# Kernel tuning notes

Hardware: AMD Instinct MI355X
Metric: run time of the kernel (lower is better)

## Reference

```python
import jax, jax.numpy as jnp
import numpy as np
import math

BS, QL, KL = 2, 2048, 2048
H, D = 16, 64          # n_heads, cell_dim
QS = KS = VS = 1024    # query/key/value feature sizes
HD = H * D


def setup_inputs() -> dict:
    key = jax.random.key(0)
    ks = jax.random.split(key, 12)
    s_in = 1.0 / math.sqrt(QS)
    s_hd = 1.0 / math.sqrt(HD)
    return {
        "query": jax.random.normal(ks[0], (BS, QL, QS), jnp.float32),
        "key": jax.random.normal(ks[1], (BS, KL, KS), jnp.float32),
        "value": jax.random.normal(ks[2], (BS, KL, VS), jnp.float32),
        # nn.Linear weights stored as [in, out] for x @ W + b
        "Wq_w": jax.random.normal(ks[3], (QS, HD), jnp.float32) * s_in,
        "Wq_b": jax.random.normal(ks[4], (HD,), jnp.float32) * s_in,
        "Wk_w": jax.random.normal(ks[5], (KS, HD), jnp.float32) * s_in,
        "Wk_b": jax.random.normal(ks[6], (HD,), jnp.float32) * s_in,
        "Wv_w": jax.random.normal(ks[7], (VS, HD), jnp.float32) * s_in,
        "Wv_b": jax.random.normal(ks[8], (HD,), jnp.float32) * s_in,
        "Wo_w": jax.random.normal(ks[9], (HD, HD), jnp.float32) * s_hd,
        "Wo_b": jax.random.normal(ks[10], (HD,), jnp.float32) * s_hd,
    }


def reference(query, key, value, Wq_w, Wq_b, Wk_w, Wk_b, Wv_w, Wv_b, Wo_w, Wo_b):
    bs, ql, _ = query.shape
    kl = key.shape[1]
    # project and split heads; torch .chunk along dim 2 == head-major reshape
    q = (query @ Wq_w + Wq_b).reshape(bs, ql, H, D).transpose(0, 2, 1, 3)  # bhqd
    k = (key @ Wk_w + Wk_b).reshape(bs, kl, H, D).transpose(0, 2, 1, 3)    # bhkd
    v = (value @ Wv_w + Wv_b).reshape(bs, kl, H, D).transpose(0, 2, 1, 3)  # bhkd
    scores = jnp.einsum("bhqd,bhkd->bhqk", q, k) / jnp.sqrt(jnp.float32(D))
    # log_softmax(...).exp() == softmax (use_mask=False path)
    w = jax.nn.softmax(scores, axis=-1)
    heads = jnp.einsum("bhqk,bhkd->bhqd", w, v)
    out = heads.transpose(0, 2, 1, 3).reshape(bs, ql, HD)  # concat heads on dim 2
    return out @ Wo_w + Wo_b
```

## Files before the change

kernel.cpp:

```cpp
#include <hip/hip_runtime.h>

#define BSZ 2
#define SEQ 2048
#define NH 16
#define DHD 64
#define HDIM 1024
#define FS 1024
#define MR (BSZ*SEQ)
#define L2E 1.4426950408889634f

typedef __bf16 bf16x8 __attribute__((ext_vector_type(8)));
typedef __bf16 bf16x2t __attribute__((ext_vector_type(2)));
typedef float f32x4 __attribute__((ext_vector_type(4)));
typedef float f32x16 __attribute__((ext_vector_type(16)));
typedef unsigned short u16;
typedef unsigned int u32;
typedef u32 u32x4 __attribute__((ext_vector_type(4)));

__device__ __forceinline__ u16 f2bf(float f) {
  u32 x = __float_as_uint(f);
  return (u16)((x + 0x7fffu + ((x >> 16) & 1u)) >> 16);
}

__device__ __forceinline__ u32 pack2bf(float a, float b) {
  bf16x2t t = {(__bf16)a, (__bf16)b};
  return __builtin_bit_cast(u32, t);
}

__device__ __forceinline__ void gload16(const void* g, void* l) {
  __builtin_amdgcn_global_load_lds(
      (const __attribute__((address_space(1))) u32*)g,
      (__attribute__((address_space(3))) u32*)l, 16, 0, 0);
}

__global__ __launch_bounds__(256) void transw4_k(
    const float* __restrict__ W0, const float* __restrict__ W1,
    const float* __restrict__ W2, const float* __restrict__ W3,
    u16* __restrict__ WTbase) {
  __shared__ float t[32][33];
  const int z = blockIdx.z;
  const float* W = z == 0 ? W0 : z == 1 ? W1 : z == 2 ? W2 : W3;
  u16* WT = WTbase + (size_t)z * FS * HDIM;
  const int tx = threadIdx.x, ty = threadIdx.y;
  const int c0 = blockIdx.x * 32, r0 = blockIdx.y * 32;
#pragma unroll
  for (int i = 0; i < 4; i++)
    t[ty + 8 * i][tx] = W[(size_t)(r0 + ty + 8 * i) * FS + c0 + tx];
  __syncthreads();
#pragma unroll
  for (int i = 0; i < 4; i++)
    WT[(size_t)(c0 + ty + 8 * i) * FS + r0 + tx] = f2bf(t[tx][ty + 8 * i]);
}

__global__ __launch_bounds__(256, 2) void gemmQKV_k(
    const float* __restrict__ qf32, const float* __restrict__ kf32,
    const float* __restrict__ vf32, const u16* __restrict__ WTbase,
    const float* __restrict__ bq, const float* __restrict__ bk,
    const float* __restrict__ bv, u16* __restrict__ QKbase,
    u16* __restrict__ VpT) {
  __shared__ u16 aL[2][128 * 64];
  __shared__ u16 bL[2][128 * 64];
  const int grp = blockIdx.y;
  const float* Af = grp == 0 ? qf32 : grp == 1 ? kf32 : vf32;
  const u16* BT = WTbase + (size_t)grp * FS * HDIM;
  const float* bias = grp == 0 ? bq : grp == 1 ? bk : bv;
  const int bx = blockIdx.x;
  const int m0 = (4 * (bx & 7) + (bx >> 6)) << 7;
  const int n0 = ((bx >> 3) & 7) << 7;
  const int tid = threadIdx.x, w = tid >> 6, lane = tid & 63;
  const int wr = ((w >> 1) << 6), wc = ((w & 1) << 6);
  const int li = lane & 15, g = lane >> 4;

  f32x4 acc[4][4];
#pragma unroll
  for (int i = 0; i < 4; i++)
#pragma unroll
    for (int j = 0; j < 4; j++) acc[i][j] = (f32x4){0.f, 0.f, 0.f, 0.f};

  const float* asrc[4];
  const u16* bsrc[4];
  int ldoff[4];
#pragma unroll
  for (int j = 0; j < 4; j++) {
    const int c = w * 4 + j;
    const int r = c * 8 + (lane >> 3);
    const int sc = (lane & 7) ^ (r & 7);
    asrc[j] = Af + (size_t)(m0 + r) * FS + sc * 8;
    bsrc[j] = BT + (size_t)(n0 + r) * FS + sc * 8;
    ldoff[j] = c * 1024;
  }

  float4 ar0[4], ar1[4];
#pragma unroll
  for (int j = 0; j < 4; j++) gload16(bsrc[j], (char*)bL[0] + ldoff[j]);
#pragma unroll
  for (int j = 0; j < 4; j++) {
    ar0[j] = *(const float4*)(asrc[j]);
    ar1[j] = *(const float4*)(asrc[j] + 4);
  }

  for (int kt = 0; kt < 16; kt++) {
    const int cur = kt & 1;
#pragma unroll
    for (int j = 0; j < 4; j++) {
      u32x4 pk;
      pk[0] = pack2bf(ar0[j].x, ar0[j].y);
      pk[1] = pack2bf(ar0[j].z, ar0[j].w);
      pk[2] = pack2bf(ar1[j].x, ar1[j].y);
      pk[3] = pack2bf(ar1[j].z, ar1[j].w);
      *(u32x4*)((char*)aL[cur] + ldoff[j] + lane * 16) = pk;
    }
    asm volatile("s_waitcnt lgkmcnt(0)" ::: "memory");
    __builtin_amdgcn_s_barrier();
    __builtin_amdgcn_sched_barrier(0);
    if (kt + 1 < 16) {
      const int ko = (kt + 1) * 64;
#pragma unroll
      for (int j = 0; j < 4; j++)
        gload16(bsrc[j] + ko, (char*)bL[cur ^ 1] + ldoff[j]);
#pragma unroll
      for (int j = 0; j < 4; j++) {
        ar0[j] = *(const float4*)(asrc[j] + ko);
        ar1[j] = *(const float4*)(asrc[j] + ko + 4);
      }
    }
    bf16x8 af[2][4], bfr[2][4];
#pragma unroll
    for (int ks = 0; ks < 2; ks++) {
#pragma unroll
      for (int mf = 0; mf < 4; mf++) {
        const int r = wr + mf * 16 + li;
        const int sl = (g + 4 * ks) ^ (r & 7);
        af[ks][mf] = *(const bf16x8*)((const char*)aL[cur] + r * 128 + sl * 16);
      }
#pragma unroll
      for (int nf = 0; nf < 4; nf++) {
        const int r = wc + nf * 16 + li;
        const int sl = (g + 4 * ks) ^ (r & 7);
        bfr[ks][nf] = *(const bf16x8*)((const char*)bL[cur] + r * 128 + sl * 16);
      }
    }
#pragma unroll
    for (int ks = 0; ks < 2; ks++)
#pragma unroll
      for (int mf = 0; mf < 4; mf++)
#pragma unroll
        for (int nf = 0; nf < 4; nf++)
          acc[mf][nf] = __builtin_amdgcn_mfma_f32_16x16x32_bf16(
              af[ks][mf], bfr[ks][nf], acc[mf][nf], 0, 0, 0);
  }

  if (grp < 2) {
    const float osc = grp == 0 ? 0.125f * L2E : 1.0f;
    u16* C = QKbase + (size_t)grp * MR * HDIM;
#pragma unroll
    for (int mf = 0; mf < 4; mf++)
#pragma unroll
      for (int nf = 0; nf < 4; nf++) {
        const int n = n0 + wc + nf * 16 + li;
        const float bvl = bias[n];
#pragma unroll
        for (int r4 = 0; r4 < 4; r4++) {
          const int m = m0 + wr + mf * 16 + g * 4 + r4;
          C[(size_t)m * HDIM + n] = f2bf((acc[mf][nf][r4] + bvl) * osc);
        }
      }
  } else {
#pragma unroll
    for (int mf = 0; mf < 4; mf++)
#pragma unroll
      for (int nf = 0; nf < 4; nf++) {
        const int n = n0 + wc + nf * 16 + li;
        const float bvl = bias[n];
        const int m = m0 + wr + mf * 16 + g * 4;
        const int bb = m >> 11, kv = m & 2047;
        ushort4 o;
        o.x = f2bf(acc[mf][nf][0] + bvl);
        o.y = f2bf(acc[mf][nf][1] + bvl);
        o.z = f2bf(acc[mf][nf][2] + bvl);
        o.w = f2bf(acc[mf][nf][3] + bvl);
        *(ushort4*)(VpT +
                    ((size_t)(bb * NH + (n >> 6)) * DHD + (n & 63)) * SEQ + kv) = o;
      }
  }
}

__global__ __launch_bounds__(256, 2) void gemm_out_k(
    const u16* __restrict__ A, const u16* __restrict__ BT,
    const float* __restrict__ bias, float* __restrict__ C) {
  __shared__ u16 aL[128 * 64];
  __shared__ u16 bL[128 * 64];
  const int bx = blockIdx.x;
  const int m0 = (4 * (bx & 7) + (bx >> 6)) << 7;
  const int n0 = ((bx >> 3) & 7) << 7;
  const int tid = threadIdx.x, w = tid >> 6, lane = tid & 63;
  const int wr = ((w >> 1) << 6), wc = ((w & 1) << 6);
  const int li = lane & 15, g = lane >> 4;

  f32x4 acc[4][4];
#pragma unroll
  for (int i = 0; i < 4; i++)
#pragma unroll
    for (int j = 0; j < 4; j++) acc[i][j] = (f32x4){0.f, 0.f, 0.f, 0.f};

  for (int k0 = 0; k0 < HDIM; k0 += 64) {
#pragma unroll
    for (int j = 0; j < 4; j++) {
      const int c = w * 4 + j;
      const int r = c * 8 + (lane >> 3);
      const int sc = (lane & 7) ^ (r & 7);
      gload16(A + (size_t)(m0 + r) * HDIM + k0 + sc * 8, (char*)aL + c * 1024);
      gload16(BT + (size_t)(n0 + r) * HDIM + k0 + sc * 8, (char*)bL + c * 1024);
    }
    __syncthreads();
    bf16x8 af[2][4], bfr[2][4];
#pragma unroll
    for (int ks = 0; ks < 2; ks++) {
#pragma unroll
      for (int mf = 0; mf < 4; mf++) {
        const int r = wr + mf * 16 + li;
        const int sl = (g + 4 * ks) ^ (r & 7);
        af[ks][mf] = *(const bf16x8*)((const char*)aL + r * 128 + sl * 16);
      }
#pragma unroll
      for (int nf = 0; nf < 4; nf++) {
        const int r = wc + nf * 16 + li;
        const int sl = (g + 4 * ks) ^ (r & 7);
        bfr[ks][nf] = *(const bf16x8*)((const char*)bL + r * 128 + sl * 16);
      }
    }
#pragma unroll
    for (int ks = 0; ks < 2; ks++)
#pragma unroll
      for (int mf = 0; mf < 4; mf++)
#pragma unroll
        for (int nf = 0; nf < 4; nf++)
          acc[mf][nf] = __builtin_amdgcn_mfma_f32_16x16x32_bf16(
              af[ks][mf], bfr[ks][nf], acc[mf][nf], 0, 0, 0);
    __syncthreads();
  }

#pragma unroll
  for (int mf = 0; mf < 4; mf++)
#pragma unroll
    for (int nf = 0; nf < 4; nf++) {
      const int n = n0 + wc + nf * 16 + li;
      const float bvl = bias[n];
#pragma unroll
      for (int r4 = 0; r4 < 4; r4++) {
        const int m = m0 + wr + mf * 16 + g * 4 + r4;
        C[(size_t)m * HDIM + n] = acc[mf][nf][r4] + bvl;
      }
    }
}

__global__ __launch_bounds__(512, 1) void attn_k(
    const u16* __restrict__ Qp, const u16* __restrict__ Kp,
    const u16* __restrict__ VpT, u16* __restrict__ Hd) {
  __shared__ u16 kbuf[4][64 * 64];
  __shared__ u16 vbuf[4][64 * 64];

  const int bid = blockIdx.x;
  const int swz = (bid & 7) * 64 + (bid >> 3);
  const int qb = swz & 15;
  const int h = (swz >> 4) & 15;
  const int b = swz >> 8;
  const int tid = threadIdx.x, w = tid >> 6, lane = tid & 63;
  const int sel = w >> 2, g3 = w & 3;
  const int q32 = lane & 31, hi = lane >> 5;
  const int q0 = qb << 7;
  const size_t qbase = (size_t)(b * SEQ + q0) * HDIM + (size_t)h * DHD;
  const size_t kbase = (size_t)(b * SEQ) * HDIM + (size_t)h * DHD;
  const size_t vtbase = (size_t)(b * NH + h) * DHD * SEQ;

  const int rr = lane >> 3;
  const int sc8 = ((lane & 7) ^ rr) * 8;
  const int fkey = (q32 & 7) << 4;

#pragma unroll
  for (int j = 0; j < 2; j++) {
    const int c = w * 2 + j;
    const int r = c * 8 + rr;
    gload16(Qp + qbase + (size_t)r * HDIM + sc8, (char*)kbuf + c * 1024);
  }
  __syncthreads();
  bf16x8 qf[4];
  {
    const char* qbp = (const char*)kbuf + (g3 * 32 + q32) * 128;
#pragma unroll
    for (int ds = 0; ds < 4; ds++)
      qf[ds] = *(const bf16x8*)(qbp + ((32 * ds + 16 * hi) ^ fkey));
  }
  __syncthreads();

  bf16x8 ones1;
#pragma unroll
  for (int i = 0; i < 8; i++) ones1[i] = (__bf16)1.0f;

  float mrun = -1e30f;
  f32x16 o0, o1, lacc;
#pragma unroll
  for (int i = 0; i < 16; i++) { o0[i] = 0.f; o1[i] = 0.f; lacc[i] = 0.f; }

  const int c0j = g3 * 2;
  const int r0r = c0j * 8 + rr;
  const u16* kp0 = Kp + kbase + (size_t)(r0r + sel * 64) * HDIM + sc8;
  const u16* kp1 = kp0 + (size_t)8 * HDIM;
  const u16* vp0 = VpT + vtbase + (size_t)r0r * SEQ + sel * 64 + sc8;
  const u16* vp1 = vp0 + (size_t)8 * SEQ;
  const int ldk0 = c0j * 1024, ldk1 = (c0j + 1) * 1024;

  auto stage2 = [&](int buf) {
    gload16(kp0, (char*)kbuf[buf] + ldk0);
    gload16(kp1, (char*)kbuf[buf] + ldk1);
    gload16(vp0, (char*)vbuf[buf] + ldk0);
    gload16(vp1, (char*)vbuf[buf] + ldk1);
    kp0 += (size_t)128 * HDIM;
    kp1 += (size_t)128 * HDIM;
    vp0 += 128;
    vp1 += 128;
  };

  stage2(sel);

#pragma unroll 1
  for (int p = 0; p < SEQ / 128; p++) {
    __syncthreads();
    if (p + 1 < SEQ / 128) stage2(sel + 2 * ((p + 1) & 1));
    const char* kl = (const char*)kbuf[sel + 2 * (p & 1)];
    const char* vl = (const char*)vbuf[sel + 2 * (p & 1)];

    f32x16 s0, s1;
#pragma unroll
    for (int i = 0; i < 16; i++) { s0[i] = 0.f; s1[i] = 0.f; }
#pragma unroll
    for (int ds = 0; ds < 4; ds++) {
      const int off = (32 * ds + 16 * hi) ^ fkey;
      const bf16x8 ka = *(const bf16x8*)(kl + q32 * 128 + off);
      const bf16x8 kb2 = *(const bf16x8*)(kl + (32 + q32) * 128 + off);
      s0 = __builtin_amdgcn_mfma_f32_32x32x16_bf16(ka, qf[ds], s0, 0, 0, 0);
      s1 = __builtin_amdgcn_mfma_f32_32x32x16_bf16(kb2, qf[ds], s1, 0, 0, 0);
    }

    float t0 = fmaxf(fmaxf(s0[0], s0[1]), s0[2]);
    float t1 = fmaxf(fmaxf(s0[3], s0[4]), s0[5]);
    float t2 = fmaxf(fmaxf(s0[6], s0[7]), s0[8]);
    float t3 = fmaxf(fmaxf(s0[9], s0[10]), s0[11]);
    float t4 = fmaxf(fmaxf(s0[12], s0[13]), s0[14]);
    float t5 = fmaxf(fmaxf(s0[15], s1[0]), s1[1]);
    float t6 = fmaxf(fmaxf(s1[2], s1[3]), s1[4]);
    float t7 = fmaxf(fmaxf(s1[5], s1[6]), s1[7]);
    float t8 = fmaxf(fmaxf(s1[8], s1[9]), s1[10]);
    float t9 = fmaxf(fmaxf(s1[11], s1[12]), s1[13]);
    float ta = fmaxf(s1[14], s1[15]);
    t0 = fmaxf(fmaxf(t0, t1), t2);
    t3 = fmaxf(fmaxf(t3, t4), t5);
    t6 = fmaxf(fmaxf(t6, t7), t8);
    t9 = fmaxf(fmaxf(t9, ta), t0);
    float mx = fmaxf(fmaxf(t3, t6), t9);
    mx = fmaxf(mx, __shfl_xor(mx, 32));
    if (!__all(mx <= mrun + 8.0f)) {
      const float mnew = fmaxf(mrun, mx);
      const float scl = __builtin_amdgcn_exp2f(mrun - mnew);
      mrun = mnew;
#pragma unroll
      for (int i = 0; i < 16; i++) {
        o0[i] *= scl; o1[i] *= scl; lacc[i] *= scl;
      }
    }
    float p0[16], p1[16];
#pragma unroll
    for (int i = 0; i < 16; i++) {
      p0[i] = __builtin_amdgcn_exp2f(s0[i] - mrun);
      p1[i] = __builtin_amdgcn_exp2f(s1[i] - mrun);
    }

#pragma unroll
    for (int kvs = 0; kvs < 4; kvs++) {
      const float* ps = (kvs < 2) ? p0 : p1;
      const int rb = (kvs & 1) * 8;
      u32 w01 = pack2bf(ps[rb + 0], ps[rb + 1]);
      u32 w23 = pack2bf(ps[rb + 2], ps[rb + 3]);
      u32 w45 = pack2bf(ps[rb + 4], ps[rb + 5]);
      u32 w67 = pack2bf(ps[rb + 6], ps[rb + 7]);
      asm("v_permlane32_swap_b32 %0, %1" : "+v"(w01), "+v"(w45));
      asm("v_permlane32_swap_b32 %0, %1" : "+v"(w23), "+v"(w67));
      u32x4 uw = {w01, w23, w45, w67};
      const bf16x8 pf = __builtin_bit_cast(bf16x8, uw);
      const int off = (32 * kvs + 16 * hi) ^ fkey;
      const bf16x8 va = *(const bf16x8*)(vl + q32 * 128 + off);
      const bf16x8 vb2 = *(const bf16x8*)(vl + (32 + q32) * 128 + off);
      o0 = __builtin_amdgcn_mfma_f32_32x32x16_bf16(va, pf, o0, 0, 0, 0);
      o1 = __builtin_amdgcn_mfma_f32_32x32x16_bf16(vb2, pf, o1, 0, 0, 0);
      lacc = __builtin_amdgcn_mfma_f32_32x32x16_bf16(ones1, pf, lacc, 0, 0, 0);
    }
  }

  const float lrun = lacc[0];

  __syncthreads();
  char* mbase = (char*)kbuf + (g3 * 64 + lane) * 144;
  if (sel == 1) {
#pragma unroll
    for (int i = 0; i < 4; i++) {
      *(f32x4*)(mbase + i * 16) =
          (f32x4){o0[4 * i], o0[4 * i + 1], o0[4 * i + 2], o0[4 * i + 3]};
      *(f32x4*)(mbase + 64 + i * 16) =
          (f32x4){o1[4 * i], o1[4 * i + 1], o1[4 * i + 2], o1[4 * i + 3]};
    }
    *(float*)(mbase + 128) = mrun;
    *(float*)(mbase + 132) = lrun;
  }
  __syncthreads();
  if (sel == 0) {
    const float m2 = *(const float*)(mbase + 128);
    const float l2 = *(const float*)(mbase + 132);
    const float ms = fmaxf(mrun, m2);
    const float f1 = __builtin_amdgcn_exp2f(mrun - ms);
    const float f2 = __builtin_amdgcn_exp2f(m2 - ms);
    const float inv = 1.f / (lrun * f1 + l2 * f2);
    const int q = q0 + g3 * 32 + q32;
    u16* orow = Hd + (size_t)(b * SEQ + q) * HDIM + (size_t)h * DHD;
#pragma unroll
    for (int rg = 0; rg < 4; rg++) {
      const f32x4 a2 = *(const f32x4*)(mbase + rg * 16);
      const f32x4 b2 = *(const f32x4*)(mbase + 64 + rg * 16);
      ushort4 ov;
      ov.x = f2bf((o0[4 * rg + 0] * f1 + a2[0] * f2) * inv);
      ov.y = f2bf((o0[4 * rg + 1] * f1 + a2[1] * f2) * inv);
      ov.z = f2bf((o0[4 * rg + 2] * f1 + a2[2] * f2) * inv);
      ov.w = f2bf((o0[4 * rg + 3] * f1 + a2[3] * f2) * inv);
      *(ushort4*)(orow + 8 * rg + 4 * hi) = ov;
      ushort4 ow;
      ow.x = f2bf((o1[4 * rg + 0] * f1 + b2[0] * f2) * inv);
      ow.y = f2bf((o1[4 * rg + 1] * f1 + b2[1] * f2) * inv);
      ow.z = f2bf((o1[4 * rg + 2] * f1 + b2[2] * f2) * inv);
      ow.w = f2bf((o1[4 * rg + 3] * f1 + b2[3] * f2) * inv);
      *(ushort4*)(orow + 32 + 8 * rg + 4 * hi) = ow;
    }
  }
}

extern "C" void kernel_launch(void* const* d_in, const int* in_sizes, int n_in,
                              void* d_out, int out_size, void* d_ws, size_t ws_size,
                              hipStream_t stream) {
  (void)in_sizes; (void)n_in; (void)out_size; (void)ws_size;
  const float* q_in = (const float*)d_in[0];
  const float* k_in = (const float*)d_in[1];
  const float* v_in = (const float*)d_in[2];
  const float* Wq_w = (const float*)d_in[3];
  const float* Wq_b = (const float*)d_in[4];
  const float* Wk_w = (const float*)d_in[5];
  const float* Wk_b = (const float*)d_in[6];
  const float* Wv_w = (const float*)d_in[7];
  const float* Wv_b = (const float*)d_in[8];
  const float* Wo_w = (const float*)d_in[9];
  const float* Wo_b = (const float*)d_in[10];

  char* ws = (char*)d_ws;
  size_t off = 0;
  auto alloc = [&](size_t n) {
    char* p = ws + off;
    off += (n + 255) & ~(size_t)255;
    return p;
  };
  u16* wT = (u16*)alloc((size_t)4 * FS * HDIM * 2);
  u16* QK = (u16*)alloc((size_t)2 * MR * HDIM * 2);
  u16* VpT = (u16*)alloc((size_t)MR * HDIM * 2);
  u16* Hdp = (u16*)alloc((size_t)MR * HDIM * 2);

  transw4_k<<<dim3(FS / 32, FS / 32, 4), dim3(32, 8), 0, stream>>>(
      Wq_w, Wk_w, Wv_w, Wo_w, wT);

  gemmQKV_k<<<dim3(256, 3), 256, 0, stream>>>(q_in, k_in, v_in, wT, Wq_b,
                                              Wk_b, Wv_b, QK, VpT);

  attn_k<<<BSZ * NH * (SEQ / 128), 512, 0, stream>>>(
      QK, QK + (size_t)MR * HDIM, VpT, Hdp);

  gemm_out_k<<<256, 256, 0, stream>>>(Hdp, wT + (size_t)3 * FS * HDIM, Wo_b,
                                      (float*)d_out);
}
```

Baseline: 138.9 us.

## Replace double-buffered LDS pipeline in QKV GEMM with single-buffered loop

The QKV projection GEMM drops its two-stage LDS double buffer. It now loads the B tile and stores the A tile into one buffer each iteration, with __syncthreads before and after the MFMA compute. This halves shared memory per block, which could allow more resident blocks, but it removes the overlap of the next B tile's global-to-LDS load with the current compute and adds a second barrier per k-step.

```diff
diff --git a/kernel.cpp b/kernel.cpp
--- a/kernel.cpp
+++ b/kernel.cpp
@@ -58,8 +58,8 @@
     const float* __restrict__ bq, const float* __restrict__ bk,
     const float* __restrict__ bv, u16* __restrict__ QKbase,
     u16* __restrict__ VpT) {
-  __shared__ u16 aL[2][128 * 64];
-  __shared__ u16 bL[2][128 * 64];
+  __shared__ u16 aL[128 * 64];
+  __shared__ u16 bL[128 * 64];
   const int grp = blockIdx.y;
   const float* Af = grp == 0 ? qf32 : grp == 1 ? kf32 : vf32;
   const u16* BT = WTbase + (size_t)grp * FS * HDIM;
@@ -78,52 +78,47 @@
     for (int j = 0; j < 4; j++) acc[i][j] = (f32x4){0.f, 0.f, 0.f, 0.f};
 
   const float* asrc[4];
-  const u16* bsrc[4];
-  int ldoff[4];
 #pragma unroll
   for (int j = 0; j < 4; j++) {
     const int c = w * 4 + j;
     const int r = c * 8 + (lane >> 3);
     const int sc = (lane & 7) ^ (r & 7);
     asrc[j] = Af + (size_t)(m0 + r) * FS + sc * 8;
-    bsrc[j] = BT + (size_t)(n0 + r) * FS + sc * 8;
-    ldoff[j] = c * 1024;
   }
 
   float4 ar0[4], ar1[4];
-#pragma unroll
-  for (int j = 0; j < 4; j++) gload16(bsrc[j], (char*)bL[0] + ldoff[j]);
 #pragma unroll
   for (int j = 0; j < 4; j++) {
     ar0[j] = *(const float4*)(asrc[j]);
     ar1[j] = *(const float4*)(asrc[j] + 4);
   }
 
-  for (int kt = 0; kt < 16; kt++) {
-    const int cur = kt & 1;
+  for (int k0 = 0; k0 < FS; k0 += 64) {
 #pragma unroll
     for (int j = 0; j < 4; j++) {
+      const int c = w * 4 + j;
+      const int r = c * 8 + (lane >> 3);
+      const int sc = (lane & 7) ^ (r & 7);
+      gload16(BT + (size_t)(n0 + r) * FS + k0 + sc * 8, (char*)bL + c * 1024);
+    }
+#pragma unroll
+    for (int j = 0; j < 4; j++) {
+      const int c = w * 4 + j;
       u32x4 pk;
       pk[0] = pack2bf(ar0[j].x, ar0[j].y);
       pk[1] = pack2bf(ar0[j].z, ar0[j].w);
       pk[2] = pack2bf(ar1[j].x, ar1[j].y);
       pk[3] = pack2bf(ar1[j].z, ar1[j].w);
-      *(u32x4*)((char*)aL[cur] + ldoff[j] + lane * 16) = pk;
-    }
-    asm volatile("s_waitcnt lgkmcnt(0)" ::: "memory");
-    __builtin_amdgcn_s_barrier();
-    __builtin_amdgcn_sched_barrier(0);
-    if (kt + 1 < 16) {
-      const int ko = (kt + 1) * 64;
-#pragma unroll
-      for (int j = 0; j < 4; j++)
-        gload16(bsrc[j] + ko, (char*)bL[cur ^ 1] + ldoff[j]);
+      *(u32x4*)((char*)aL + c * 1024 + lane * 16) = pk;
+    }
+    if (k0 + 64 < FS) {
 #pragma unroll
       for (int j = 0; j < 4; j++) {
-        ar0[j] = *(const float4*)(asrc[j] + ko);
-        ar1[j] = *(const float4*)(asrc[j] + ko + 4);
-      }
-    }
+        ar0[j] = *(const float4*)(asrc[j] + k0 + 64);
+        ar1[j] = *(const float4*)(asrc[j] + k0 + 68);
+      }
+    }
+    __syncthreads();
     bf16x8 af[2][4], bfr[2][4];
 #pragma unroll
     for (int ks = 0; ks < 2; ks++) {
@@ -131,13 +126,13 @@
       for (int mf = 0; mf < 4; mf++) {
         const int r = wr + mf * 16 + li;
         const int sl = (g + 4 * ks) ^ (r & 7);
-        af[ks][mf] = *(const bf16x8*)((const char*)aL[cur] + r * 128 + sl * 16);
+        af[ks][mf] = *(const bf16x8*)((const char*)aL + r * 128 + sl * 16);
       }
 #pragma unroll
       for (int nf = 0; nf < 4; nf++) {
         const int r = wc + nf * 16 + li;
         const int sl = (g + 4 * ks) ^ (r & 7);
-        bfr[ks][nf] = *(const bf16x8*)((const char*)bL[cur] + r * 128 + sl * 16);
+        bfr[ks][nf] = *(const bf16x8*)((const char*)bL + r * 128 + sl * 16);
       }
     }
 #pragma unroll
@@ -148,6 +143,7 @@
         for (int nf = 0; nf < 4; nf++)
           acc[mf][nf] = __builtin_amdgcn_mfma_f32_16x16x32_bf16(
               af[ks][mf], bfr[ks][nf], acc[mf][nf], 0, 0, 0);
+    __syncthreads();
   }
 
   if (grp < 2) {
```

New measurement: 122.0 us. -12.2%, faster.
